# Performance work log

Hardware: AMD Instinct MI355X
Metric: run time of the kernel (lower is better)

## Reference

```python
import jax, jax.numpy as jnp
import numpy as np

N_NODES = 100000
N_CELLS = 200000
N_EDGES = 300000
D = 128            # input_size == attention_size
HID = 128          # hidden width of custom_func MLP
SCALE = np.sqrt(np.float32(D))


def segment_softmax(src, seg_ids, num_segments):
    # src: [M, 1], seg_ids: [M] -> softmax normalized within each segment
    m = jax.ops.segment_max(src, seg_ids, num_segments=num_segments)
    e = jnp.exp(src - m[seg_ids])
    s = jax.ops.segment_sum(e, seg_ids, num_segments=num_segments)
    return e / s[seg_ids]


def setup_inputs() -> dict:
    key = jax.random.key(0)
    ks = jax.random.split(key, 9)
    cell_attr = jax.random.normal(ks[0], (N_CELLS, D), dtype=jnp.float32)
    edge_attr = jax.random.normal(ks[1], (N_EDGES, D), dtype=jnp.float32)
    node_embedding = jax.random.normal(ks[2], (N_NODES, D), dtype=jnp.float32)
    edge_index = jax.random.randint(ks[3], (2, N_EDGES), 0, N_NODES, dtype=jnp.int32)
    face = jax.random.randint(ks[4], (3, N_CELLS), 0, N_NODES, dtype=jnp.int32)
    # custom_func: 2-layer MLP (2D -> HID -> D)
    W1 = jax.random.normal(ks[5], (2 * D, HID), dtype=jnp.float32) / np.sqrt(2 * D)
    b1 = jnp.zeros((HID,), dtype=jnp.float32)
    W2 = jax.random.normal(ks[6], (HID, D), dtype=jnp.float32) / np.sqrt(HID)
    b2 = jnp.zeros((D,), dtype=jnp.float32)
    return {"cell_attr": cell_attr, "edge_attr": edge_attr,
            "node_embedding": node_embedding, "edge_index": edge_index,
            "face": face, "W1": W1, "b1": b1, "W2": W2, "b2": b2}


def reference(cell_attr, edge_attr, node_embedding, edge_index, face, W1, b1, W2, b2):
    senders, receivers = edge_index[0], edge_index[1]
    two_out = jnp.concatenate([receivers, senders], axis=0)   # outdegree order [2E]
    two_edge = jnp.concatenate([edge_attr, edge_attr], axis=0)  # [2E, D]

    # attention over edges grouped by target (outdegree) node
    att_src = jnp.sum(two_edge * node_embedding[two_out], axis=1, keepdims=True) / SCALE
    att = segment_softmax(att_src, two_out, N_NODES)            # [2E, 1]
    node_agg = jax.ops.segment_sum(two_edge * att, two_out, num_segments=N_NODES)  # [N, D]

    # cells gather mean of their 3 nodes
    cell_agg = (node_agg[face[0]] + node_agg[face[1]] + node_agg[face[2]]) / 3.0  # [C, D]

    # custom_func MLP on cat(cell_attr, cell_agg)
    h = jax.nn.relu(jnp.concatenate([cell_attr, cell_agg], axis=1) @ W1 + b1)
    cell_attr_new = h @ W2 + b2                                  # [C, D]

    # scatter_mean of cell features back to nodes
    cells_node_index = jnp.concatenate([face[0], face[1], face[2]], axis=0)  # [3C]
    tripled = jnp.concatenate([cell_attr_new] * 3, axis=0)                   # [3C, D]
    sums = jax.ops.segment_sum(tripled, cells_node_index, num_segments=N_NODES)
    counts = jax.ops.segment_sum(jnp.ones((3 * N_CELLS,), jnp.float32),
                                 cells_node_index, num_segments=N_NODES)
    node_attr = sums / jnp.maximum(counts, 1.0)[:, None]

    return cell_attr_new, node_attr
```

## Files before the change

### kernel.cpp

```cpp
#include <hip/hip_runtime.h>

#define NN 100000
#define NC 200000
#define NE 300000
#define D  128
#define NB 391
#define ATT_B 2048
#define HB 2344

typedef unsigned short u16;
typedef __attribute__((ext_vector_type(8))) short bf16x8;
typedef __attribute__((ext_vector_type(4))) float f32x4;

__device__ __forceinline__ u16 f2bf(float x) {
    unsigned int u = __float_as_uint(x);
    u += 0x7fffu + ((u >> 16) & 1u);
    return (u16)(u >> 16);
}
__device__ __forceinline__ float bf2f(u16 h) {
    return __uint_as_float((unsigned int)h << 16);
}
__device__ __forceinline__ unsigned int cvt_pk_bf16(float a, float b) {
    unsigned int r;
    asm("v_cvt_pk_bf16_f32 %0, %1, %2" : "=v"(r) : "v"(a), "v"(b));
    return r;
}

#define MFMA16(a, b, c) __builtin_amdgcn_mfma_f32_16x16x32_bf16((a), (b), (c), 0, 0, 0)

__global__ __launch_bounds__(256) void k_att_prep(const float* __restrict__ edge_attr,
                                                  const float* __restrict__ emb,
                                                  const int* __restrict__ ei,
                                                  const int* __restrict__ face,
                                                  float* __restrict__ expv,
                                                  float* __restrict__ denom,
                                                  int* __restrict__ cntA,
                                                  int* __restrict__ cntF,
                                                  const float* __restrict__ W1,
                                                  const float* __restrict__ W2,
                                                  u16* __restrict__ w1h, u16* __restrict__ w1l,
                                                  u16* __restrict__ w2h, u16* __restrict__ w2l) {
    int b = blockIdx.x;
    int t = threadIdx.x;
    if (b < ATT_B) {
        const int HW = ATT_B * 8;
        int hw  = b * 8 + (t >> 5);
        int sub = t & 31;
        const float inv_scale = 0.08838834764831845f;
        for (int e0 = hw; e0 < NE; e0 += 2 * HW) {
            int e1 = e0 + HW;
            bool h1 = (e1 < NE);
            int sd0 = ei[e0], rc0 = ei[NE + e0];
            int sd1 = h1 ? ei[e1] : 0;
            int rc1 = h1 ? ei[NE + e1] : 0;
            float4 a0 = ((const float4*)(edge_attr + (size_t)e0 * D))[sub];
            float4 r0 = ((const float4*)(emb + (size_t)rc0 * D))[sub];
            float4 s0 = ((const float4*)(emb + (size_t)sd0 * D))[sub];
            float dr0 = a0.x * r0.x + a0.y * r0.y + a0.z * r0.z + a0.w * r0.w;
            float ds0 = a0.x * s0.x + a0.y * s0.y + a0.z * s0.z + a0.w * s0.w;
            float dr1 = 0.f, ds1 = 0.f;
            if (h1) {
                float4 a1 = ((const float4*)(edge_attr + (size_t)e1 * D))[sub];
                float4 r1 = ((const float4*)(emb + (size_t)rc1 * D))[sub];
                float4 s1 = ((const float4*)(emb + (size_t)sd1 * D))[sub];
                dr1 = a1.x * r1.x + a1.y * r1.y + a1.z * r1.z + a1.w * r1.w;
                ds1 = a1.x * s1.x + a1.y * s1.y + a1.z * s1.z + a1.w * s1.w;
            }
            #pragma unroll
            for (int off = 16; off > 0; off >>= 1) {
                dr0 += __shfl_xor(dr0, off);
                ds0 += __shfl_xor(ds0, off);
                dr1 += __shfl_xor(dr1, off);
                ds1 += __shfl_xor(ds1, off);
            }
            if (sub == 0) {
                float er = __expf(dr0 * inv_scale);
                float es = __expf(ds0 * inv_scale);
                expv[e0] = er;
                expv[NE + e0] = es;
                atomicAdd(&denom[rc0], er);
                atomicAdd(&denom[sd0], es);
                if (h1) {
                    float er1 = __expf(dr1 * inv_scale);
                    float es1 = __expf(ds1 * inv_scale);
                    expv[e1] = er1;
                    expv[NE + e1] = es1;
                    atomicAdd(&denom[rc1], er1);
                    atomicAdd(&denom[sd1], es1);
                }
            }
        }
    } else if (b < ATT_B + HB) {
        int i = (b - ATT_B) * 256 + t;
        if (i >= 2 * NE) return;
        int tgt = (i < NE) ? ei[NE + i] : ei[i - NE];
        atomicAdd(&cntA[tgt], 1);
    } else if (b < ATT_B + 2 * HB) {
        int i = (b - ATT_B - HB) * 256 + t;
        if (i >= 3 * NC) return;
        atomicAdd(&cntF[face[i]], 1);
    } else {
        int tid = (b - ATT_B - 2 * HB) * 256 + t;
        if (tid >= 6144) return;
        int l = tid & 63;
        int f = tid >> 6;
        const float* W; u16 *oh, *ol; int fi;
        if (f < 64) { W = W1; oh = w1h; ol = w1l; fi = f; }
        else        { W = W2; oh = w2h; ol = w2l; fi = f - 64; }
        int kt = fi >> 3, nt = fi & 7;
        int k0 = kt * 32 + 8 * (l >> 4);
        int n  = nt * 16 + (l & 15);
        #pragma unroll
        for (int i = 0; i < 8; i++) {
            float x = W[(size_t)(k0 + i) * 128 + n];
            u16 h = f2bf(x);
            oh[(size_t)fi * 512 + l * 8 + i] = h;
            ol[(size_t)fi * 512 + l * 8 + i] = f2bf(x - bf2f(h));
        }
    }
}

__global__ __launch_bounds__(256) void k_scan_blocks(const int* __restrict__ cntA,
                                                     const int* __restrict__ cntF,
                                                     int* __restrict__ bsumA,
                                                     int* __restrict__ bsumF) {
    __shared__ int s[256];
    int bb = blockIdx.x;
    bool fa = bb >= NB;
    const int* cnt = fa ? cntF : cntA;
    int* bsum = fa ? bsumF : bsumA;
    int blk = fa ? bb - NB : bb;
    int t = threadIdx.x;
    int i = blk * 256 + t;
    s[t] = (i < NN) ? cnt[i] : 0;
    __syncthreads();
    #pragma unroll
    for (int off = 128; off > 0; off >>= 1) {
        if (t < off) s[t] += s[t + off];
        __syncthreads();
    }
    if (t == 0) bsum[blk] = s[0];
}

__global__ __launch_bounds__(512) void k_scan_top(int* __restrict__ bsumA,
                                                  int* __restrict__ bsumF, int nb) {
    __shared__ int s[512];
    int* bsum = blockIdx.x ? bsumF : bsumA;
    int t = threadIdx.x;
    int v = (t < nb) ? bsum[t] : 0;
    s[t] = v;
    __syncthreads();
    #pragma unroll
    for (int off = 1; off < 512; off <<= 1) {
        int x = (t >= off) ? s[t - off] : 0;
        __syncthreads();
        s[t] += x;
        __syncthreads();
    }
    if (t < nb) bsum[t] = s[t] - v;
}

__global__ __launch_bounds__(256) void k_scan_final(const int* __restrict__ cntA,
                                                    const int* __restrict__ cntF,
                                                    const int* __restrict__ bsumA,
                                                    const int* __restrict__ bsumF,
                                                    int* __restrict__ offA,
                                                    int* __restrict__ offF) {
    __shared__ int s[256];
    int bb = blockIdx.x;
    bool fa = bb >= NB;
    const int* cnt = fa ? cntF : cntA;
    const int* bsum = fa ? bsumF : bsumA;
    int* off_out = fa ? offF : offA;
    int total = fa ? 3 * NC : 2 * NE;
    int blk = fa ? bb - NB : bb;
    int t = threadIdx.x;
    int i = blk * 256 + t;
    int v = (i < NN) ? cnt[i] : 0;
    s[t] = v;
    __syncthreads();
    #pragma unroll
    for (int off = 1; off < 256; off <<= 1) {
        int x = (t >= off) ? s[t - off] : 0;
        __syncthreads();
        s[t] += x;
        __syncthreads();
    }
    if (i < NN) off_out[i] = s[t] - v + bsum[blk];
    if (i == 0) off_out[NN] = total;
}

__global__ __launch_bounds__(256) void k_fill(const int* __restrict__ ei,
                                              const float* __restrict__ expv,
                                              const int* __restrict__ face,
                                              const int* __restrict__ offA,
                                              const int* __restrict__ offF,
                                              int* __restrict__ curA,
                                              int* __restrict__ curF,
                                              int2* __restrict__ swA,
                                              int* __restrict__ slotsF) {
    int b = blockIdx.x;
    int t = threadIdx.x;
    if (b < HB) {
        int i = b * 256 + t;
        if (i >= 2 * NE) return;
        int tgt = (i < NE) ? ei[NE + i] : ei[i - NE];
        int pos = offA[tgt] + atomicAdd(&curA[tgt], 1);
        int2 p;
        p.x = (i < NE) ? i : i - NE;
        p.y = __float_as_int(expv[i]);
        swA[pos] = p;
    } else {
        int i = (b - HB) * 256 + t;
        if (i >= 3 * NC) return;
        int tgt = face[i];
        int pos = offF[tgt] + atomicAdd(&curF[tgt], 1);
        int c = i; if (c >= NC) c -= NC; if (c >= NC) c -= NC;
        slotsF[pos] = c;
    }
}

__global__ __launch_bounds__(256) void k_agg_gather(const float* __restrict__ edge_attr,
                                                    const int2* __restrict__ swA,
                                                    const float* __restrict__ denom,
                                                    const int* __restrict__ offs,
                                                    float* __restrict__ na) {
    int n = blockIdx.x * 4 + (threadIdx.x >> 6);
    int lane = threadIdx.x & 63;
    if (n >= NN) return;
    int s0 = offs[n], s1 = offs[n + 1];
    int deg = s1 - s0;
    float2 acc = {0.f, 0.f};
    int base = 0;
    while (base < deg) {
        int chunk = deg - base;
        if (chunk > 64) chunk = 64;
        int sl = 0; float wl = 0.f;
        if (lane < chunk) {
            int2 p = swA[s0 + base + lane];
            sl = p.x;
            wl = __int_as_float(p.y);
        }
        int j = 0;
        for (; j + 4 <= chunk; j += 4) {
            int r0 = __shfl(sl, j),     r1 = __shfl(sl, j + 1);
            int r2 = __shfl(sl, j + 2), r3 = __shfl(sl, j + 3);
            float w0 = __shfl(wl, j),     w1 = __shfl(wl, j + 1);
            float w2 = __shfl(wl, j + 2), w3 = __shfl(wl, j + 3);
            float2 a0 = ((const float2*)(edge_attr + (size_t)r0 * D))[lane];
            float2 a1 = ((const float2*)(edge_attr + (size_t)r1 * D))[lane];
            float2 a2 = ((const float2*)(edge_attr + (size_t)r2 * D))[lane];
            float2 a3 = ((const float2*)(edge_attr + (size_t)r3 * D))[lane];
            acc.x += w0 * a0.x + w1 * a1.x + w2 * a2.x + w3 * a3.x;
            acc.y += w0 * a0.y + w1 * a1.y + w2 * a2.y + w3 * a3.y;
        }
        for (; j < chunk; ++j) {
            int rr = __shfl(sl, j);
            float ww = __shfl(wl, j);
            float2 a = ((const float2*)(edge_attr + (size_t)rr * D))[lane];
            acc.x += ww * a.x;
            acc.y += ww * a.y;
        }
        base += chunk;
    }
    float inv = (deg > 0) ? 1.f / denom[n] : 0.f;
    float2 r; r.x = acc.x * inv; r.y = acc.y * inv;
    ((float2*)(na + (size_t)n * D))[lane] = r;
}

__global__ __launch_bounds__(256) void k_smean_gather(const float* __restrict__ cell_out,
                                                      const int* __restrict__ offs,
                                                      const int* __restrict__ slots,
                                                      float* __restrict__ node_out) {
    int n = blockIdx.x * 4 + (threadIdx.x >> 6);
    int lane = threadIdx.x & 63;
    if (n >= NN) return;
    int s0 = offs[n], s1 = offs[n + 1];
    int deg = s1 - s0;
    float2 acc = {0.f, 0.f};
    int base = 0;
    while (base < deg) {
        int chunk = deg - base;
        if (chunk > 64) chunk = 64;
        int sl = 0;
        if (lane < chunk) sl = slots[s0 + base + lane];
        int j = 0;
        for (; j + 4 <= chunk; j += 4) {
            int c0 = __shfl(sl, j),     c1 = __shfl(sl, j + 1);
            int c2 = __shfl(sl, j + 2), c3 = __shfl(sl, j + 3);
            float2 y0 = ((const float2*)(cell_out + (size_t)c0 * D))[lane];
            float2 y1 = ((const float2*)(cell_out + (size_t)c1 * D))[lane];
            float2 y2 = ((const float2*)(cell_out + (size_t)c2 * D))[lane];
            float2 y3 = ((const float2*)(cell_out + (size_t)c3 * D))[lane];
            acc.x += y0.x + y1.x + y2.x + y3.x;
            acc.y += y0.y + y1.y + y2.y + y3.y;
        }
        for (; j < chunk; ++j) {
            int cc = __shfl(sl, j);
            float2 y = ((const float2*)(cell_out + (size_t)cc * D))[lane];
            acc.x += y.x;
            acc.y += y.y;
        }
        base += chunk;
    }
    float inv = deg ? 1.f / (float)deg : 0.f;
    float2 r; r.x = acc.x * inv; r.y = acc.y * inv;
    ((float2*)(node_out + (size_t)n * D))[lane] = r;
}

__device__ __forceinline__ void stage_split(char* lds, int row, int col8, const float* v) {
    unsigned int byte = ((unsigned int)row << 9) + ((unsigned int)col8 << 4);
    byte ^= (unsigned int)(row & 7) << 4;
    uint4 hi, lo;
    unsigned int* hp = (unsigned int*)&hi;
    unsigned int* lp = (unsigned int*)&lo;
    #pragma unroll
    for (int i = 0; i < 4; i++) {
        unsigned int h = cvt_pk_bf16(v[2 * i], v[2 * i + 1]);
        float h0 = __uint_as_float(h << 16);
        float h1 = __uint_as_float(h & 0xffff0000u);
        hp[i] = h;
        lp[i] = cvt_pk_bf16(v[2 * i] - h0, v[2 * i + 1] - h1);
    }
    *(uint4*)(lds + byte)         = hi;
    *(uint4*)(lds + 16384 + byte) = lo;
}

__global__ __launch_bounds__(256, 4) void k_mlp(const float* __restrict__ cell_attr,
                                                const float* __restrict__ na,
                                                const int* __restrict__ face,
                                                const u16* __restrict__ w1h,
                                                const u16* __restrict__ w1l,
                                                const u16* __restrict__ w2h,
                                                const u16* __restrict__ w2l,
                                                const float* __restrict__ b1,
                                                const float* __restrict__ b2,
                                                float* __restrict__ out) {
    __shared__ char lds[32768];
    const int t  = threadIdx.x;
    const int c0 = blockIdx.x * 32;

    {
        const int r = t >> 3;
        const int q = t & 7;
        float v[16];
        const float* pa = cell_attr + (size_t)(c0 + r) * D + q * 16;
        #pragma unroll
        for (int i = 0; i < 4; i++) *(float4*)(v + 4 * i) = *(const float4*)(pa + 4 * i);
        stage_split(lds, r, q * 2,     v);
        stage_split(lds, r, q * 2 + 1, v + 8);

        const int cid = c0 + r;
        const int f0 = face[cid], f1 = face[NC + cid], f2 = face[2 * NC + cid];
        const float* p0 = na + (size_t)f0 * D + q * 16;
        const float* p1 = na + (size_t)f1 * D + q * 16;
        const float* p2 = na + (size_t)f2 * D + q * 16;
        const float third = 1.f / 3.f;
        #pragma unroll
        for (int i = 0; i < 4; i++) {
            float4 a0 = *(const float4*)(p0 + 4 * i);
            float4 a1 = *(const float4*)(p1 + 4 * i);
            float4 a2 = *(const float4*)(p2 + 4 * i);
            v[4 * i + 0] = (a0.x + a1.x + a2.x) * third;
            v[4 * i + 1] = (a0.y + a1.y + a2.y) * third;
            v[4 * i + 2] = (a0.z + a1.z + a2.z) * third;
            v[4 * i + 3] = (a0.w + a1.w + a2.w) * third;
        }
        stage_split(lds, r, 16 + q * 2, v);
        stage_split(lds, r, 17 + q * 2, v + 8);
    }
    __syncthreads();

    const int w  = t >> 6;
    const int l  = t & 63;
    const int lr = l & 15;
    const int lg = l >> 4;
    const unsigned int swz = (unsigned int)(lr & 7) << 4;
    const size_t wl8 = (size_t)l * 8;
    const f32x4 z4 = {0.f, 0.f, 0.f, 0.f};
    f32x4 acc[2][2] = {{z4, z4}, {z4, z4}};

    {
        const unsigned int abase = ((unsigned int)lr << 9) + ((unsigned int)lg << 4);
        const u16* pW1h = w1h + (size_t)(w * 2) * 512 + wl8;
        const u16* pW1l = w1l + (size_t)(w * 2) * 512 + wl8;
        #pragma unroll 2
        for (int kt = 0; kt < 8; ++kt) {
            unsigned int ab = (abase + (unsigned int)kt * 64) ^ swz;
            bf16x8 aH0 = *(const bf16x8*)(lds + ab);
            bf16x8 aL0 = *(const bf16x8*)(lds + 16384 + ab);
            bf16x8 aH1 = *(const bf16x8*)(lds + ab + 8192);
            bf16x8 aL1 = *(const bf16x8*)(lds + 16384 + ab + 8192);
            #pragma unroll
            for (int jn = 0; jn < 2; ++jn) {
                size_t fo = (size_t)(kt * 8 + jn) * 512;
                bf16x8 bH = *(const bf16x8*)(pW1h + fo);
                bf16x8 bL = *(const bf16x8*)(pW1l + fo);
                acc[0][jn] = MFMA16(aH0, bL, acc[0][jn]);
                acc[0][jn] = MFMA16(aL0, bH, acc[0][jn]);
                acc[0][jn] = MFMA16(aH0, bH, acc[0][jn]);
                acc[1][jn] = MFMA16(aH1, bL, acc[1][jn]);
                acc[1][jn] = MFMA16(aL1, bH, acc[1][jn]);
                acc[1][jn] = MFMA16(aH1, bH, acc[1][jn]);
            }
        }
    }

    __syncthreads();

    {
        const int col0 = w * 32 + lr;
        const int col1 = col0 + 16;
        const float bb0 = b1[col0];
        const float bb1 = b1[col1];
        #pragma unroll
        for (int rt = 0; rt < 2; ++rt) {
            #pragma unroll
            for (int r = 0; r < 4; ++r) {
                int row = rt * 16 + lg * 4 + r;
                float h0 = fmaxf(acc[rt][0][r] + bb0, 0.f);
                float h1 = fmaxf(acc[rt][1][r] + bb1, 0.f);
                unsigned int ph = cvt_pk_bf16(h0, h1);
                float f0 = __uint_as_float(ph << 16);
                float f1 = __uint_as_float(ph & 0xffff0000u);
                unsigned int pl = cvt_pk_bf16(h0 - f0, h1 - f1);
                unsigned int swzr = (unsigned int)(row & 7) << 4;
                unsigned int b0 = (((unsigned int)row << 8) + ((unsigned int)col0 << 1)) ^ swzr;
                unsigned int bcol1 = (((unsigned int)row << 8) + ((unsigned int)col1 << 1)) ^ swzr;
                *(u16*)(lds + b0)            = (u16)ph;
                *(u16*)(lds + bcol1)         = (u16)(ph >> 16);
                *(u16*)(lds + 8192 + b0)     = (u16)pl;
                *(u16*)(lds + 8192 + bcol1)  = (u16)(pl >> 16);
            }
        }
    }
    __syncthreads();

    f32x4 acc2[2][2] = {{z4, z4}, {z4, z4}};
    {
        const unsigned int abase = ((unsigned int)lr << 8) + ((unsigned int)lg << 4);
        const u16* pW2h = w2h + (size_t)(w * 2) * 512 + wl8;
        const u16* pW2l = w2l + (size_t)(w * 2) * 512 + wl8;
        #pragma unroll 2
        for (int kt = 0; kt < 4; ++kt) {
            unsigned int ab = (abase + (unsigned int)kt * 64) ^ swz;
            bf16x8 aH0 = *(const bf16x8*)(lds + ab);
            bf16x8 aL0 = *(const bf16x8*)(lds + 8192 + ab);
            bf16x8 aH1 = *(const bf16x8*)(lds + ab + 4096);
            bf16x8 aL1 = *(const bf16x8*)(lds + 8192 + ab + 4096);
            #pragma unroll
            for (int jn = 0; jn < 2; ++jn) {
                size_t fo = (size_t)(kt * 8 + jn) * 512;
                bf16x8 bH = *(const bf16x8*)(pW2h + fo);
                bf16x8 bL = *(const bf16x8*)(pW2l + fo);
                acc2[0][jn] = MFMA16(aH0, bL, acc2[0][jn]);
                acc2[0][jn] = MFMA16(aL0, bH, acc2[0][jn]);
                acc2[0][jn] = MFMA16(aH0, bH, acc2[0][jn]);
                acc2[1][jn] = MFMA16(aH1, bL, acc2[1][jn]);
                acc2[1][jn] = MFMA16(aL1, bH, acc2[1][jn]);
                acc2[1][jn] = MFMA16(aH1, bH, acc2[1][jn]);
            }
        }
    }

    #pragma unroll
    for (int jn = 0; jn < 2; ++jn) {
        int col = w * 32 + jn * 16 + lr;
        float bb = b2[col];
        #pragma unroll
        for (int rt = 0; rt < 2; ++rt) {
            #pragma unroll
            for (int r = 0; r < 4; ++r) {
                int row = c0 + rt * 16 + lg * 4 + r;
                out[(size_t)row * D + col] = acc2[rt][jn][r] + bb;
            }
        }
    }
}

extern "C" void kernel_launch(void* const* d_in, const int* in_sizes, int n_in,
                              void* d_out, int out_size, void* d_ws, size_t ws_size,
                              hipStream_t stream) {
    (void)in_sizes; (void)n_in; (void)out_size; (void)ws_size;
    const float* cell_attr = (const float*)d_in[0];
    const float* edge_attr = (const float*)d_in[1];
    const float* emb       = (const float*)d_in[2];
    const int*   ei        = (const int*)d_in[3];
    const int*   face      = (const int*)d_in[4];
    const float* W1        = (const float*)d_in[5];
    const float* b1        = (const float*)d_in[6];
    const float* W2        = (const float*)d_in[7];
    const float* b2        = (const float*)d_in[8];

    float* out_cell = (float*)d_out;
    float* out_node = out_cell + (size_t)NC * D;

    float* denom  = (float*)d_ws;
    int*   cntA   = (int*)d_ws + NN;
    int*   cntF   = cntA + NN;
    int*   curA   = cntF + NN;
    int*   curF   = curA + NN;
    float* expv   = (float*)(curF + NN);
    int*   offA   = (int*)(expv + 2 * NE);
    int*   offF   = offA + NN + 1;
    int*   bsumA  = offF + NN + 1;
    int*   bsumF  = bsumA + 512;
    int*   slotsF = bsumF + 512;
    int2*  swA    = (int2*)(((uintptr_t)(slotsF + 3 * NC) + 7) & ~(uintptr_t)7);
    u16* w1h = (u16*)(((uintptr_t)(swA + 2 * NE) + 15) & ~(uintptr_t)15);
    u16* w1l = w1h + 64 * 512;
    u16* w2h = w1l + 64 * 512;
    u16* w2l = w2h + 32 * 512;

    hipMemsetAsync(d_ws, 0, (size_t)5 * NN * 4, stream);

    k_att_prep<<<ATT_B + 2 * HB + 24, 256, 0, stream>>>(edge_attr, emb, ei, face, expv, denom,
                                                        cntA, cntF, W1, W2, w1h, w1l, w2h, w2l);

    k_scan_blocks<<<2 * NB, 256, 0, stream>>>(cntA, cntF, bsumA, bsumF);
    k_scan_top   <<<2, 512, 0, stream>>>(bsumA, bsumF, NB);
    k_scan_final <<<2 * NB, 256, 0, stream>>>(cntA, cntF, bsumA, bsumF, offA, offF);

    k_fill<<<2 * HB, 256, 0, stream>>>(ei, expv, face, offA, offF, curA, curF, swA, slotsF);

    k_agg_gather<<<(NN + 3) / 4, 256, 0, stream>>>(edge_attr, swA, denom, offA, out_node);

    k_mlp<<<NC / 32, 256, 0, stream>>>(cell_attr, out_node, face,
                                       w1h, w1l, w2h, w2l, b1, b2, out_cell);

    k_smean_gather<<<(NN + 3) / 4, 256, 0, stream>>>(out_cell, offF, slotsF, out_node);
}
```

Baseline: 665.8 us.

## Compute softmax denominator in gather and fold degree counting into attention kernel

The float atomic accumulation of softmax denominators is removed; the aggregation gather now sums the exp weights it already loads for each node and reduces them across the wavefront. Edge-degree counting moves into the attention loop as integer atomics, which drops the separate counting blocks. The combined prep kernel is split into an attention kernel and a face/weight prep kernel launched one after the other, so those two parts no longer overlap within a single launch. The memset also shrinks by one array.

New measurement: 658.1 us. No clear change (-1.2%).

```diff
diff --git a/kernel.cpp b/kernel.cpp
--- a/kernel.cpp
+++ b/kernel.cpp
@@ -28,79 +28,70 @@
 
 #define MFMA16(a, b, c) __builtin_amdgcn_mfma_f32_16x16x32_bf16((a), (b), (c), 0, 0, 0)
 
-__global__ __launch_bounds__(256) void k_att_prep(const float* __restrict__ edge_attr,
-                                                  const float* __restrict__ emb,
-                                                  const int* __restrict__ ei,
-                                                  const int* __restrict__ face,
-                                                  float* __restrict__ expv,
-                                                  float* __restrict__ denom,
-                                                  int* __restrict__ cntA,
-                                                  int* __restrict__ cntF,
-                                                  const float* __restrict__ W1,
-                                                  const float* __restrict__ W2,
-                                                  u16* __restrict__ w1h, u16* __restrict__ w1l,
-                                                  u16* __restrict__ w2h, u16* __restrict__ w2l) {
+__global__ __launch_bounds__(256) void k_att(const float* __restrict__ edge_attr,
+                                             const float* __restrict__ emb,
+                                             const int* __restrict__ ei,
+                                             float* __restrict__ expv,
+                                             int* __restrict__ cntA) {
+    const int HW = ATT_B * 8;
+    int hw  = blockIdx.x * 8 + (threadIdx.x >> 5);
+    int sub = threadIdx.x & 31;
+    const float inv_scale = 0.08838834764831845f;
+    for (int e0 = hw; e0 < NE; e0 += 2 * HW) {
+        int e1 = e0 + HW;
+        bool h1 = (e1 < NE);
+        int sd0 = ei[e0], rc0 = ei[NE + e0];
+        int sd1 = h1 ? ei[e1] : 0;
+        int rc1 = h1 ? ei[NE + e1] : 0;
+        float4 a0 = ((const float4*)(edge_attr + (size_t)e0 * D))[sub];
+        float4 r0 = ((const float4*)(emb + (size_t)rc0 * D))[sub];
+        float4 s0 = ((const float4*)(emb + (size_t)sd0 * D))[sub];
+        float dr0 = a0.x * r0.x + a0.y * r0.y + a0.z * r0.z + a0.w * r0.w;
+        float ds0 = a0.x * s0.x + a0.y * s0.y + a0.z * s0.z + a0.w * s0.w;
+        float dr1 = 0.f, ds1 = 0.f;
+        if (h1) {
+            float4 a1 = ((const float4*)(edge_attr + (size_t)e1 * D))[sub];
+            float4 r1 = ((const float4*)(emb + (size_t)rc1 * D))[sub];
+            float4 s1 = ((const float4*)(emb + (size_t)sd1 * D))[sub];
+            dr1 = a1.x * r1.x + a1.y * r1.y + a1.z * r1.z + a1.w * r1.w;
+            ds1 = a1.x * s1.x + a1.y * s1.y + a1.z * s1.z + a1.w * s1.w;
+        }
+        #pragma unroll
+        for (int off = 16; off > 0; off >>= 1) {
+            dr0 += __shfl_xor(dr0, off);
+            ds0 += __shfl_xor(ds0, off);
+            dr1 += __shfl_xor(dr1, off);
+            ds1 += __shfl_xor(ds1, off);
+        }
+        if (sub == 0) {
+            expv[e0]      = __expf(dr0 * inv_scale);
+            expv[NE + e0] = __expf(ds0 * inv_scale);
+            atomicAdd(&cntA[rc0], 1);
+            atomicAdd(&cntA[sd0], 1);
+            if (h1) {
+                expv[e1]      = __expf(dr1 * inv_scale);
+                expv[NE + e1] = __expf(ds1 * inv_scale);
+                atomicAdd(&cntA[rc1], 1);
+                atomicAdd(&cntA[sd1], 1);
+            }
+        }
+    }
+}
+
+__global__ __launch_bounds__(256) void k_prep_face_w(const int* __restrict__ face,
+                                                     int* __restrict__ cntF,
+                                                     const float* __restrict__ W1,
+                                                     const float* __restrict__ W2,
+                                                     u16* __restrict__ w1h, u16* __restrict__ w1l,
+                                                     u16* __restrict__ w2h, u16* __restrict__ w2l) {
     int b = blockIdx.x;
     int t = threadIdx.x;
-    if (b < ATT_B) {
-        const int HW = ATT_B * 8;
-        int hw  = b * 8 + (t >> 5);
-        int sub = t & 31;
-        const float inv_scale = 0.08838834764831845f;
-        for (int e0 = hw; e0 < NE; e0 += 2 * HW) {
-            int e1 = e0 + HW;
-            bool h1 = (e1 < NE);
-            int sd0 = ei[e0], rc0 = ei[NE + e0];
-            int sd1 = h1 ? ei[e1] : 0;
-            int rc1 = h1 ? ei[NE + e1] : 0;
-            float4 a0 = ((const float4*)(edge_attr + (size_t)e0 * D))[sub];
-            float4 r0 = ((const float4*)(emb + (size_t)rc0 * D))[sub];
-            float4 s0 = ((const float4*)(emb + (size_t)sd0 * D))[sub];
-            float dr0 = a0.x * r0.x + a0.y * r0.y + a0.z * r0.z + a0.w * r0.w;
-            float ds0 = a0.x * s0.x + a0.y * s0.y + a0.z * s0.z + a0.w * s0.w;
-            float dr1 = 0.f, ds1 = 0.f;
-            if (h1) {
-                float4 a1 = ((const float4*)(edge_attr + (size_t)e1 * D))[sub];
-                float4 r1 = ((const float4*)(emb + (size_t)rc1 * D))[sub];
-                float4 s1 = ((const float4*)(emb + (size_t)sd1 * D))[sub];
-                dr1 = a1.x * r1.x + a1.y * r1.y + a1.z * r1.z + a1.w * r1.w;
-                ds1 = a1.x * s1.x + a1.y * s1.y + a1.z * s1.z + a1.w * s1.w;
-            }
-            #pragma unroll
-            for (int off = 16; off > 0; off >>= 1) {
-                dr0 += __shfl_xor(dr0, off);
-                ds0 += __shfl_xor(ds0, off);
-                dr1 += __shfl_xor(dr1, off);
-                ds1 += __shfl_xor(ds1, off);
-            }
-            if (sub == 0) {
-                float er = __expf(dr0 * inv_scale);
-                float es = __expf(ds0 * inv_scale);
-                expv[e0] = er;
-                expv[NE + e0] = es;
-                atomicAdd(&denom[rc0], er);
-                atomicAdd(&denom[sd0], es);
-                if (h1) {
-                    float er1 = __expf(dr1 * inv_scale);
-                    float es1 = __expf(ds1 * inv_scale);
-                    expv[e1] = er1;
-                    expv[NE + e1] = es1;
-                    atomicAdd(&denom[rc1], er1);
-                    atomicAdd(&denom[sd1], es1);
-                }
-            }
-        }
-    } else if (b < ATT_B + HB) {
-        int i = (b - ATT_B) * 256 + t;
-        if (i >= 2 * NE) return;
-        int tgt = (i < NE) ? ei[NE + i] : ei[i - NE];
-        atomicAdd(&cntA[tgt], 1);
-    } else if (b < ATT_B + 2 * HB) {
-        int i = (b - ATT_B - HB) * 256 + t;
+    if (b < HB) {
+        int i = b * 256 + t;
         if (i >= 3 * NC) return;
         atomicAdd(&cntF[face[i]], 1);
     } else {
-        int tid = (b - ATT_B - 2 * HB) * 256 + t;
+        int tid = (b - HB) * 256 + t;
         if (tid >= 6144) return;
         int l = tid & 63;
         int f = tid >> 6;
@@ -222,7 +213,6 @@
 
 __global__ __launch_bounds__(256) void k_agg_gather(const float* __restrict__ edge_attr,
                                                     const int2* __restrict__ swA,
-                                                    const float* __restrict__ denom,
                                                     const int* __restrict__ offs,
                                                     float* __restrict__ na) {
     int n = blockIdx.x * 4 + (threadIdx.x >> 6);
@@ -231,6 +221,7 @@
     int s0 = offs[n], s1 = offs[n + 1];
     int deg = s1 - s0;
     float2 acc = {0.f, 0.f};
+    float wsum = 0.f;
     int base = 0;
     while (base < deg) {
         int chunk = deg - base;
@@ -241,6 +232,7 @@
             sl = p.x;
             wl = __int_as_float(p.y);
         }
+        wsum += wl;
         int j = 0;
         for (; j + 4 <= chunk; j += 4) {
             int r0 = __shfl(sl, j),     r1 = __shfl(sl, j + 1);
@@ -263,7 +255,9 @@
         }
         base += chunk;
     }
-    float inv = (deg > 0) ? 1.f / denom[n] : 0.f;
+    #pragma unroll
+    for (int off = 32; off > 0; off >>= 1) wsum += __shfl_xor(wsum, off);
+    float inv = (deg > 0) ? 1.f / wsum : 0.f;
     float2 r; r.x = acc.x * inv; r.y = acc.y * inv;
     ((float2*)(na + (size_t)n * D))[lane] = r;
 }
@@ -303,7 +297,8 @@
         }
         base += chunk;
     }
-    float inv = deg ? 1.f / (float)deg : 0.f;
+    int degc = s1 - s0;
+    float inv = degc ? 1.f / (float)degc : 0.f;
     float2 r; r.x = acc.x * inv; r.y = acc.y * inv;
     ((float2*)(node_out + (size_t)n * D))[lane] = r;
 }
@@ -495,8 +490,7 @@
     float* out_cell = (float*)d_out;
     float* out_node = out_cell + (size_t)NC * D;
 
-    float* denom  = (float*)d_ws;
-    int*   cntA   = (int*)d_ws + NN;
+    int*   cntA   = (int*)d_ws;
     int*   cntF   = cntA + NN;
     int*   curA   = cntF + NN;
     int*   curF   = curA + NN;
@@ -512,10 +506,11 @@
     u16* w2h = w1l + 64 * 512;
     u16* w2l = w2h + 32 * 512;
 
-    hipMemsetAsync(d_ws, 0, (size_t)5 * NN * 4, stream);
-
-    k_att_prep<<<ATT_B + 2 * HB + 24, 256, 0, stream>>>(edge_attr, emb, ei, face, expv, denom,
-                                                        cntA, cntF, W1, W2, w1h, w1l, w2h, w2l);
+    hipMemsetAsync(d_ws, 0, (size_t)4 * NN * 4, stream);
+
+    k_att<<<ATT_B, 256, 0, stream>>>(edge_attr, emb, ei, expv, cntA);
+
+    k_prep_face_w<<<HB + 24, 256, 0, stream>>>(face, cntF, W1, W2, w1h, w1l, w2h, w2l);
 
     k_scan_blocks<<<2 * NB, 256, 0, stream>>>(cntA, cntF, bsumA, bsumF);
     k_scan_top   <<<2, 512, 0, stream>>>(bsumA, bsumF, NB);
@@ -523,7 +518,7 @@
 
     k_fill<<<2 * HB, 256, 0, stream>>>(ei, expv, face, offA, offF, curA, curF, swA, slotsF);
 
-    k_agg_gather<<<(NN + 3) / 4, 256, 0, stream>>>(edge_attr, swA, denom, offA, out_node);
+    k_agg_gather<<<(NN + 3) / 4, 256, 0, stream>>>(edge_attr, swA, offA, out_node);
 
     k_mlp<<<NC / 32, 256, 0, stream>>>(cell_attr, out_node, face,
                                        w1h, w1l, w2h, w2l, b1, b2, out_cell);
```
